# Performance work log

Measured on AMD Instinct MI355X. Metric: run time of the kernel, lower is better.

The kernel has to match this reference:

```python
import jax, jax.numpy as jnp
import numpy as np

NUM_DATA, MAX_SEQ_LEN, NUM_INPUTS = 256, 2048, 256
NUM_HIDDEN, NUM_OUTPUTS = 1024, 256

def _xavier(key, shape):
    fan_in, fan_out = shape
    limit = float(np.sqrt(6.0 / (fan_in + fan_out)))
    return jax.random.uniform(key, shape, jnp.float32, -limit, limit)

def setup_inputs() -> dict:
    key = jax.random.key(0)
    ks = jax.random.split(key, 8)
    return {
        "x": jax.random.normal(ks[0], (NUM_DATA, MAX_SEQ_LEN, NUM_INPUTS), jnp.float32),
        "W_in1": _xavier(ks[1], (NUM_INPUTS, NUM_HIDDEN)),
        "b_in1": jnp.zeros((NUM_HIDDEN,), jnp.float32),
        "W_rec1": _xavier(ks[2], (NUM_HIDDEN, NUM_HIDDEN)),
        "W_in2": _xavier(ks[3], (NUM_INPUTS, NUM_HIDDEN)),
        "b_in2": jnp.zeros((NUM_HIDDEN,), jnp.float32),
        "W_rec2": _xavier(ks[4], (NUM_HIDDEN, NUM_HIDDEN)),
        "W_out": _xavier(ks[5], (NUM_HIDDEN, NUM_OUTPUTS)),
        "b_out": jnp.zeros((NUM_OUTPUTS,), jnp.float32),
    }

def reference(x, W_in1, b_in1, W_rec1, W_in2, b_in2, W_rec2, W_out, b_out):
    num_data, max_seq_len, _ = x.shape
    num_hidden = W_in1.shape[1]

    def step_fn(carry, inp):
        z1, z2 = carry                      # each [max_seq_len, num_hidden]
        x_seq, step = inp                   # x_seq: [max_seq_len, num_inputs]
        z12 = z1 + z2
        z1_new = jnp.tanh(x_seq @ W_in1 + z12 @ W_rec1 + b_in1)
        z2_cand = jnp.tanh(x_seq @ W_in2 + z2 @ W_rec2 + b_in2)
        # Layer2 holds previous state on odd steps
        z2_new = jnp.where((step % 2) == 1, z2, z2_cand)
        z_out = jnp.tanh(z1_new @ W_out + b_out)[-1, :]  # [num_outputs]
        return (z1_new, z2_new), z_out

    z0 = jnp.zeros((max_seq_len, num_hidden), x.dtype)
    steps = jnp.arange(num_data)
    _, out = jax.lax.scan(step_fn, (z0, z0), (x, steps))
    return out  # [num_data, num_outputs]
```

## Files before the change

kernel.cpp:

```cpp
#include <hip/hip_runtime.h>
#include <math.h>

#define ND  256
#define SEQ 2048
#define NI  256
#define NH  1024
#define NO  256

#define RB   64
#define RT   1024
#define HPB  16
#define NHP  (NH + 1)

#define XTB  32
#define OTB  8

typedef unsigned long long u64;

#define AL64(p)    __hip_atomic_load((p), __ATOMIC_RELAXED, __HIP_MEMORY_SCOPE_AGENT)
#define AS64(p,v)  __hip_atomic_store((p), (v), __ATOMIC_RELAXED, __HIP_MEMORY_SCOPE_AGENT)

__global__ void xproj(const float* __restrict__ x,
                      const float* __restrict__ Win1, const float* __restrict__ b1,
                      const float* __restrict__ Win2, const float* __restrict__ b2,
                      float* __restrict__ X1, float* __restrict__ X2) {
    const int   layer = blockIdx.z;
    const int   t0    = blockIdx.y * XTB;
    const int   h     = blockIdx.x * 256 + threadIdx.x;
    const float* W = layer ? Win2 : Win1;
    const float* b = layer ? b2   : b1;
    float*       X = layer ? X2   : X1;

    __shared__ float lx[XTB][NI];
    for (int idx = threadIdx.x; idx < XTB * NI; idx += 256) {
        int r = idx >> 8, c = idx & (NI - 1);
        lx[r][c] = x[(size_t)(t0 + r) * SEQ * NI + (size_t)(SEQ - 1) * NI + c];
    }
    __syncthreads();

    float acc[XTB];
    float bias = b[h];
    #pragma unroll
    for (int r = 0; r < XTB; ++r) acc[r] = bias;

    for (int i = 0; i < NI; ++i) {
        float wv = W[i * NH + h];
        #pragma unroll
        for (int r = 0; r < XTB; ++r) acc[r] += lx[r][i] * wv;
    }
    #pragma unroll
    for (int r = 0; r < XTB; ++r) X[(t0 + r) * NH + h] = acc[r];
}

__launch_bounds__(RT, 1)
__global__ void recur(const float* __restrict__ Wr1, const float* __restrict__ Wr2,
                      const float* __restrict__ X1,  const float* __restrict__ X2,
                      u64* Z12, u64* Z2, float* Z1hist) {
    __shared__ float lW1[HPB][NHP];
    __shared__ float lW2[HPB][NHP];
    __shared__ float sz [2][NH];
    __shared__ float sz2[2][NH];

    const int tid = threadIdx.x;
    const int h0  = blockIdx.x * HPB;

    for (int idx = tid; idx < HPB * NH; idx += RT) {
        int hw = idx & (HPB - 1);
        int k  = idx >> 4;
        lW1[hw][k] = Wr1[(size_t)k * NH + h0 + hw];
        lW2[hw][k] = Wr2[(size_t)k * NH + h0 + hw];
    }
    __syncthreads();

    const int w = tid >> 6;
    const int l = tid & 63;
    const int h = h0 + w;

    float z2h = 0.0f;

    for (int t = 0; t < ND; ++t) {
        const bool even = (t & 1) == 0;
        const int  q    = t >> 1;

        float xv1 = X1[t * NH + h];
        float xv2 = even ? X2[t * NH + h] : 0.0f;

        const u64* p1 = Z12 + (t & 1) * NH + tid;
        u64 v1 = AL64(p1);
        u64 v2 = 0;
        const u64* p2 = Z2 + (q & 1) * NH + tid;
        if (even) v2 = AL64(p2);
        while ((unsigned)(v1 >> 32) != (unsigned)t) v1 = AL64(p1);
        sz[t & 1][tid] = __uint_as_float((unsigned)v1);
        if (even) {
            while ((unsigned)(v2 >> 32) != (unsigned)q) v2 = AL64(p2);
            sz2[q & 1][tid] = __uint_as_float((unsigned)v2);
        }
        __syncthreads();

        float r1 = 0.0f, r2 = 0.0f;
        #pragma unroll
        for (int j = 0; j < 16; ++j) {
            int k = l + 64 * j;
            r1 += sz[t & 1][k] * lW1[w][k];
        }
        if (even) {
            #pragma unroll
            for (int j = 0; j < 16; ++j) {
                int k = l + 64 * j;
                r2 += sz2[q & 1][k] * lW2[w][k];
            }
        }
        #pragma unroll
        for (int off = 32; off; off >>= 1) r1 += __shfl_xor(r1, off, 64);
        if (even) {
            #pragma unroll
            for (int off = 32; off; off >>= 1) r2 += __shfl_xor(r2, off, 64);
        }

        if (l == 0) {
            float z1n = tanhf(xv1 + r1);
            if (even) z2h = tanhf(xv2 + r2);
            Z1hist[t * NH + h] = z1n;
            u64 o1 = ((u64)(unsigned)(t + 1) << 32) | (u64)__float_as_uint(z1n + z2h);
            AS64(Z12 + ((t + 1) & 1) * NH + h, o1);
            if (even) {
                u64 o2 = ((u64)(unsigned)(q + 1) << 32) | (u64)__float_as_uint(z2h);
                AS64(Z2 + ((q + 1) & 1) * NH + h, o2);
            }
        }
    }
}

__global__ void outproj(const float* __restrict__ Z1hist,
                        const float* __restrict__ Wout,
                        const float* __restrict__ bout,
                        float* __restrict__ out) {
    const int t0 = blockIdx.x * OTB;
    const int o  = threadIdx.x;

    __shared__ float lz[OTB][NH];
    for (int idx = threadIdx.x; idx < OTB * NH; idx += 256) {
        int r = idx >> 10, c = idx & (NH - 1);
        lz[r][c] = Z1hist[(t0 + r) * NH + c];
    }
    __syncthreads();

    float acc[OTB];
    float bias = bout[o];
    #pragma unroll
    for (int r = 0; r < OTB; ++r) acc[r] = bias;

    for (int hh = 0; hh < NH; ++hh) {
        float wv = Wout[hh * NO + o];
        #pragma unroll
        for (int r = 0; r < OTB; ++r) acc[r] += lz[r][hh] * wv;
    }
    #pragma unroll
    for (int r = 0; r < OTB; ++r) out[(t0 + r) * NO + o] = tanhf(acc[r]);
}

extern "C" void kernel_launch(void* const* d_in, const int* in_sizes, int n_in,
                              void* d_out, int out_size, void* d_ws, size_t ws_size,
                              hipStream_t stream) {
    const float* x     = (const float*)d_in[0];
    const float* Win1  = (const float*)d_in[1];
    const float* b1    = (const float*)d_in[2];
    const float* Wr1   = (const float*)d_in[3];
    const float* Win2  = (const float*)d_in[4];
    const float* b2    = (const float*)d_in[5];
    const float* Wr2   = (const float*)d_in[6];
    const float* Wout  = (const float*)d_in[7];
    const float* bout  = (const float*)d_in[8];
    float* out = (float*)d_out;

    u64*   Z12 = (u64*)d_ws;
    u64*   Z2  = Z12 + 2 * NH;
    float* Z1h = (float*)(Z2 + 2 * NH);
    float* X1  = Z1h + ND * NH;
    float* X2  = X1 + ND * NH;

    hipMemsetAsync(Z12, 0, 4 * NH * sizeof(u64), stream);

    dim3 xg(NH / 256, ND / XTB, 2);
    xproj<<<xg, 256, 0, stream>>>(x, Win1, b1, Win2, b2, X1, X2);

    recur<<<RB, RT, 0, stream>>>(Wr1, Wr2, X1, X2, Z12, Z2, Z1h);

    outproj<<<ND / OTB, NO, 0, stream>>>(Z1h, Wout, bout, out);
}
```

Measured before the change: 1.832 ms.

## Replace per-element tagged state polling with per-block flag barrier

Drops the 64-bit values that packed a step tag with each hidden state, along with the spin by every thread on its own element. Each block now publishes a step counter flag after its state stores drain. Wave 0 of every block polls the other blocks' flags before reading plain float state. This halves state traffic and concentrates polling on 63 lanes, but adds a serial store-then-flag round trip, an extra block barrier per step, and moves the X1 loads after the wait. It relies on relaxed atomics plus a waitcnt for memory ordering.

Result: faster. 1.586 ms (-13.4%).

```diff
diff --git a/kernel.cpp b/kernel.cpp
--- a/kernel.cpp
+++ b/kernel.cpp
@@ -15,10 +15,8 @@
 #define XTB  32
 #define OTB  8
 
-typedef unsigned long long u64;
-
-#define AL64(p)    __hip_atomic_load((p), __ATOMIC_RELAXED, __HIP_MEMORY_SCOPE_AGENT)
-#define AS64(p,v)  __hip_atomic_store((p), (v), __ATOMIC_RELAXED, __HIP_MEMORY_SCOPE_AGENT)
+#define ALF(p)   __hip_atomic_load((p), __ATOMIC_RELAXED, __HIP_MEMORY_SCOPE_AGENT)
+#define ASF(p,v) __hip_atomic_store((p), (v), __ATOMIC_RELAXED, __HIP_MEMORY_SCOPE_AGENT)
 
 __global__ void xproj(const float* __restrict__ x,
                       const float* __restrict__ Win1, const float* __restrict__ b1,
@@ -55,14 +53,15 @@
 __launch_bounds__(RT, 1)
 __global__ void recur(const float* __restrict__ Wr1, const float* __restrict__ Wr2,
                       const float* __restrict__ X1,  const float* __restrict__ X2,
-                      u64* Z12, u64* Z2, float* Z1hist) {
+                      float* Z12, float* Z2, float* Z1hist, int* flags) {
     __shared__ float lW1[HPB][NHP];
     __shared__ float lW2[HPB][NHP];
     __shared__ float sz [2][NH];
     __shared__ float sz2[2][NH];
 
     const int tid = threadIdx.x;
-    const int h0  = blockIdx.x * HPB;
+    const int b   = blockIdx.x;
+    const int h0  = b * HPB;
 
     for (int idx = tid; idx < HPB * NH; idx += RT) {
         int hw = idx & (HPB - 1);
@@ -82,20 +81,21 @@
         const bool even = (t & 1) == 0;
         const int  q    = t >> 1;
 
-        float xv1 = X1[t * NH + h];
-        float xv2 = even ? X2[t * NH + h] : 0.0f;
+        if (t != 0 && w == 0 && l != b) {
+            const int* fp = flags + l * 32;
+            while (ALF(fp) < t) { }
+        }
+        __syncthreads();
 
-        const u64* p1 = Z12 + (t & 1) * NH + tid;
-        u64 v1 = AL64(p1);
-        u64 v2 = 0;
-        const u64* p2 = Z2 + (q & 1) * NH + tid;
-        if (even) v2 = AL64(p2);
-        while ((unsigned)(v1 >> 32) != (unsigned)t) v1 = AL64(p1);
-        sz[t & 1][tid] = __uint_as_float((unsigned)v1);
+        float xv1  = X1[t * NH + h];
+        float z12v = ALF(Z12 + (t & 1) * NH + tid);
+        float xv2 = 0.0f, z2v = 0.0f;
         if (even) {
-            while ((unsigned)(v2 >> 32) != (unsigned)q) v2 = AL64(p2);
-            sz2[q & 1][tid] = __uint_as_float((unsigned)v2);
+            xv2 = X2[t * NH + h];
+            z2v = ALF(Z2 + (q & 1) * NH + tid);
         }
+        sz[t & 1][tid] = z12v;
+        if (even) sz2[q & 1][tid] = z2v;
         __syncthreads();
 
         float r1 = 0.0f, r2 = 0.0f;
@@ -122,13 +122,15 @@
             float z1n = tanhf(xv1 + r1);
             if (even) z2h = tanhf(xv2 + r2);
             Z1hist[t * NH + h] = z1n;
-            u64 o1 = ((u64)(unsigned)(t + 1) << 32) | (u64)__float_as_uint(z1n + z2h);
-            AS64(Z12 + ((t + 1) & 1) * NH + h, o1);
-            if (even) {
-                u64 o2 = ((u64)(unsigned)(q + 1) << 32) | (u64)__float_as_uint(z2h);
-                AS64(Z2 + ((q + 1) & 1) * NH + h, o2);
-            }
+            ASF(Z12 + ((t + 1) & 1) * NH + h, z1n + z2h);
+            if (even) ASF(Z2 + (((q + 1) & 1)) * NH + h, z2h);
         }
+
+        if (t == ND - 1) break;
+
+        __builtin_amdgcn_s_waitcnt(0);
+        __syncthreads();
+        if (tid == 0) ASF(flags + b * 32, t + 1);
     }
 }
 
@@ -174,18 +176,20 @@
     const float* bout  = (const float*)d_in[8];
     float* out = (float*)d_out;
 
-    u64*   Z12 = (u64*)d_ws;
-    u64*   Z2  = Z12 + 2 * NH;
-    float* Z1h = (float*)(Z2 + 2 * NH);
-    float* X1  = Z1h + ND * NH;
-    float* X2  = X1 + ND * NH;
+    float* ws    = (float*)d_ws;
+    float* Z12   = ws;
+    float* Z2    = Z12 + 2 * NH;
+    int*   flags = (int*)(Z2 + 2 * NH);
+    float* Z1h   = (float*)(flags + RB * 32);
+    float* X1    = Z1h + ND * NH;
+    float* X2    = X1 + ND * NH;
 
-    hipMemsetAsync(Z12, 0, 4 * NH * sizeof(u64), stream);
+    hipMemsetAsync(Z12, 0, (4 * NH) * sizeof(float) + RB * 32 * sizeof(int), stream);
 
     dim3 xg(NH / 256, ND / XTB, 2);
     xproj<<<xg, 256, 0, stream>>>(x, Win1, b1, Win2, b2, X1, X2);
 
-    recur<<<RB, RT, 0, stream>>>(Wr1, Wr2, X1, X2, Z12, Z2, Z1h);
+    recur<<<RB, RT, 0, stream>>>(Wr1, Wr2, X1, X2, Z12, Z2, Z1h, flags);
 
     outproj<<<ND / OTB, NO, 0, stream>>>(Z1h, Wout, bout, out);
 }
```

## Publish z1 and z2 separately and batch-poll flags with wave-wide any

Applied to the files above, without the earlier changes.

The recurrent kernel now publishes z1 and z2 as separate tagged values and forms z1+z2 on the consumer side during the dot product. Layer-2 state is fetched on odd steps, so even steps only wait on layer-1 flags. The spin loop checks all flags with a wave-wide vote and sleeps between polls to reduce memory traffic, and the final step skips publishing. This adds an extra shared-memory read per element in the layer-1 dot product, and the sleep can add wake-up latency on the critical path.

Result: slower. 1.909 ms (+4.2%).

```diff
diff --git a/kernel.cpp b/kernel.cpp
--- a/kernel.cpp
+++ b/kernel.cpp
@@ -17,8 +17,8 @@
 
 typedef unsigned long long u64;
 
-#define AL64(p)    __hip_atomic_load((p), __ATOMIC_RELAXED, __HIP_MEMORY_SCOPE_AGENT)
-#define AS64(p,v)  __hip_atomic_store((p), (v), __ATOMIC_RELAXED, __HIP_MEMORY_SCOPE_AGENT)
+#define AL64(p)   __hip_atomic_load((p), __ATOMIC_RELAXED, __HIP_MEMORY_SCOPE_AGENT)
+#define AS64(p,v) __hip_atomic_store((p), (v), __ATOMIC_RELAXED, __HIP_MEMORY_SCOPE_AGENT)
 
 __global__ void xproj(const float* __restrict__ x,
                       const float* __restrict__ Win1, const float* __restrict__ b1,
@@ -55,14 +55,15 @@
 __launch_bounds__(RT, 1)
 __global__ void recur(const float* __restrict__ Wr1, const float* __restrict__ Wr2,
                       const float* __restrict__ X1,  const float* __restrict__ X2,
-                      u64* Z12, u64* Z2, float* Z1hist) {
+                      u64* Z1b, u64* Z2b, float* Z1hist) {
     __shared__ float lW1[HPB][NHP];
     __shared__ float lW2[HPB][NHP];
-    __shared__ float sz [2][NH];
+    __shared__ float sz1[2][NH];
     __shared__ float sz2[2][NH];
 
     const int tid = threadIdx.x;
-    const int h0  = blockIdx.x * HPB;
+    const int b   = blockIdx.x;
+    const int h0  = b * HPB;
 
     for (int idx = tid; idx < HPB * NH; idx += RT) {
         int hw = idx & (HPB - 1);
@@ -76,57 +77,64 @@
     const int l = tid & 63;
     const int h = h0 + w;
 
-    float z2h = 0.0f;
-
     for (int t = 0; t < ND; ++t) {
-        const bool even = (t & 1) == 0;
-        const int  q    = t >> 1;
+        const bool even   = (t & 1) == 0;
+        const int  q      = t >> 1;
+        const bool stage2 = (t == 0) || !even;
+        const int  rd2    = (t == 0) ? 0 : (even ? (q & 1) : ((q + 1) & 1));
+        const unsigned e2 = (t == 0) ? 0u : (unsigned)(q + 1);
 
         float xv1 = X1[t * NH + h];
         float xv2 = even ? X2[t * NH + h] : 0.0f;
 
-        const u64* p1 = Z12 + (t & 1) * NH + tid;
+        const u64* p1 = Z1b + (t & 1) * NH + tid;
+        const u64* p2 = Z2b + rd2 * NH + tid;
         u64 v1 = AL64(p1);
-        u64 v2 = 0;
-        const u64* p2 = Z2 + (q & 1) * NH + tid;
-        if (even) v2 = AL64(p2);
-        while ((unsigned)(v1 >> 32) != (unsigned)t) v1 = AL64(p1);
-        sz[t & 1][tid] = __uint_as_float((unsigned)v1);
-        if (even) {
-            while ((unsigned)(v2 >> 32) != (unsigned)q) v2 = AL64(p2);
-            sz2[q & 1][tid] = __uint_as_float((unsigned)v2);
+        u64 v2 = stage2 ? AL64(p2) : 0;
+        for (;;) {
+            bool bad = ((unsigned)(v1 >> 32) != (unsigned)t) ||
+                       (stage2 && ((unsigned)(v2 >> 32) != e2));
+            if (!__any(bad)) break;
+            __builtin_amdgcn_s_sleep(1);
+            v1 = AL64(p1);
+            if (stage2) v2 = AL64(p2);
         }
+        sz1[t & 1][tid] = __uint_as_float((unsigned)v1);
+        if (stage2) sz2[rd2][tid] = __uint_as_float((unsigned)v2);
         __syncthreads();
 
+        const float* z1c = sz1[t & 1];
+        const float* z2c = sz2[rd2];
         float r1 = 0.0f, r2 = 0.0f;
         #pragma unroll
         for (int j = 0; j < 16; ++j) {
             int k = l + 64 * j;
-            r1 += sz[t & 1][k] * lW1[w][k];
+            r1 += (z1c[k] + z2c[k]) * lW1[w][k];
         }
         if (even) {
             #pragma unroll
             for (int j = 0; j < 16; ++j) {
                 int k = l + 64 * j;
-                r2 += sz2[q & 1][k] * lW2[w][k];
+                r2 += z2c[k] * lW2[w][k];
             }
         }
         #pragma unroll
-        for (int off = 32; off; off >>= 1) r1 += __shfl_xor(r1, off, 64);
-        if (even) {
-            #pragma unroll
-            for (int off = 32; off; off >>= 1) r2 += __shfl_xor(r2, off, 64);
+        for (int off = 32; off; off >>= 1) {
+            r1 += __shfl_xor(r1, off, 64);
+            if (even) r2 += __shfl_xor(r2, off, 64);
         }
 
         if (l == 0) {
             float z1n = tanhf(xv1 + r1);
-            if (even) z2h = tanhf(xv2 + r2);
             Z1hist[t * NH + h] = z1n;
-            u64 o1 = ((u64)(unsigned)(t + 1) << 32) | (u64)__float_as_uint(z1n + z2h);
-            AS64(Z12 + ((t + 1) & 1) * NH + h, o1);
-            if (even) {
-                u64 o2 = ((u64)(unsigned)(q + 1) << 32) | (u64)__float_as_uint(z2h);
-                AS64(Z2 + ((q + 1) & 1) * NH + h, o2);
+            if (t < ND - 1) {
+                u64 o1 = ((u64)(unsigned)(t + 1) << 32) | (u64)__float_as_uint(z1n);
+                AS64(Z1b + ((t + 1) & 1) * NH + h, o1);
+                if (even) {
+                    float z2h = tanhf(xv2 + r2);
+                    u64 o2 = ((u64)(unsigned)(q + 1) << 32) | (u64)__float_as_uint(z2h);
+                    AS64(Z2b + ((q + 1) & 1) * NH + h, o2);
+                }
             }
         }
     }
@@ -174,18 +182,18 @@
     const float* bout  = (const float*)d_in[8];
     float* out = (float*)d_out;
 
-    u64*   Z12 = (u64*)d_ws;
-    u64*   Z2  = Z12 + 2 * NH;
-    float* Z1h = (float*)(Z2 + 2 * NH);
+    u64*   Z1b = (u64*)d_ws;
+    u64*   Z2b = Z1b + 2 * NH;
+    float* Z1h = (float*)(Z2b + 2 * NH);
     float* X1  = Z1h + ND * NH;
     float* X2  = X1 + ND * NH;
 
-    hipMemsetAsync(Z12, 0, 4 * NH * sizeof(u64), stream);
+    hipMemsetAsync(Z1b, 0, 4 * NH * sizeof(u64), stream);
 
     dim3 xg(NH / 256, ND / XTB, 2);
     xproj<<<xg, 256, 0, stream>>>(x, Win1, b1, Win2, b2, X1, X2);
 
-    recur<<<RB, RT, 0, stream>>>(Wr1, Wr2, X1, X2, Z12, Z2, Z1h);
+    recur<<<RB, RT, 0, stream>>>(Wr1, Wr2, X1, X2, Z1b, Z2b, Z1h);
 
     outproj<<<ND / OTB, NO, 0, stream>>>(Z1h, Wout, bout, out);
 }
```
